# Kernel tuning notes

Hardware: AMD Instinct MI355X
Metric: run time of the kernel (lower is better)

## Reference

```python
import jax, jax.numpy as jnp
import numpy as np

RHO = 1.0


def _cayley():
    # Geometric-product structure constants for Cl(2,0), basis (1, e1, e2, e12).
    C = np.zeros((4, 4, 4), dtype=np.float32)
    entries = [
        (0, 0, 0, 1), (0, 1, 1, 1), (0, 2, 2, 1), (0, 3, 3, 1),
        (1, 0, 1, 1), (1, 1, 0, 1), (1, 2, 3, 1), (1, 3, 2, 1),
        (2, 0, 2, 1), (2, 1, 3, -1), (2, 2, 0, 1), (2, 3, 1, -1),
        (3, 0, 3, 1), (3, 1, 2, -1), (3, 2, 1, 1), (3, 3, 0, -1),
    ]
    for x, y, z, s in entries:
        C[x, y, z] = s
    return jnp.asarray(C)

CAYLEY = _cayley()

B, I, O, G, X = 64, 64, 64, 4096, 4
GRID_MIN, GRID_MAX = -2.0, 2.0


def setup_inputs() -> dict:
    key = jax.random.key(0)
    k1, k2, k3 = jax.random.split(key, 3)
    x = jax.random.normal(k1, (B, I, X), dtype=jnp.float32)
    # random_grid: quasirandom points in [grid_min, grid_max]^X (Sobol in torch; uniform here)
    grid = jax.random.uniform(k2, (G, X), dtype=jnp.float32) * (GRID_MAX - GRID_MIN) + GRID_MIN
    weights = jax.random.normal(k3, (I, O, G, X), dtype=jnp.float32)
    silu_weight = jnp.ones((I, O, X), dtype=jnp.float32)
    silu_bias = jnp.zeros((I, O, X), dtype=jnp.float32)
    return {"x": x, "grid": grid, "weights": weights,
            "silu_weight": silu_weight, "silu_bias": silu_bias}


def reference(x, grid, weights, silu_weight, silu_bias):
    # x: (B, I, X); grid: (G, X); weights: (I, O, G, X)
    diff = x[:, :, None, :] - grid[None, None, :, :]          # (B, I, G, X)
    # algebra.norm(v)**2 with Euclidean metric = sum over multivector components
    rbf = jnp.exp(-jnp.sum(diff * diff, axis=-1) / RHO)       # (B, I, G)
    result = jnp.einsum('big,iogx->biox', rbf, weights)       # (B, I, O, X)
    # componentwise SiLU branch: geometric product via cayley tensor
    sx = jax.nn.silu(x)                                       # (B, I, X)
    silu_val = jnp.einsum('iox,biy,xyz->bioz', silu_weight, sx, CAYLEY)
    silu_val = silu_val + silu_bias                           # broadcast (B, I, O, X)
    out = jnp.sum(result + silu_val, axis=1)                  # 'biox->box'
    return out                                                # NoNorm: identity norm
```

## Files before the change

kernel.cpp:

```cpp
#include <hip/hip_runtime.h>
#include <hip/hip_bf16.h>

#define BB 64
#define II 64
#define OO 64
#define GG 4096
#define KP 32
#define NCH 8
#define GC (GG / NCH)
#define NPH (GC / KP)

typedef short bf16x8 __attribute__((ext_vector_type(8)));
typedef short bf16x4 __attribute__((ext_vector_type(4)));
typedef float f32x4  __attribute__((ext_vector_type(4)));

static __device__ __forceinline__ short f2bf(float f) {
    __hip_bfloat16 h = __float2bfloat16(f);
    return __builtin_bit_cast(short, h);
}

__global__ __launch_bounds__(512, 4)
void kan_main(const float* __restrict__ xg, const float* __restrict__ grd,
              const float* __restrict__ wts, float* __restrict__ dst,
              int atomic_mode)
{
    __shared__ __align__(16) float          Wst[2][OO * KP * 4];
    __shared__ __align__(16) unsigned short As [2][BB * KP];
    __shared__ __align__(16) float4         Gs [GC];

    const int i  = blockIdx.x;
    const int ch = blockIdx.y;
    const int g0 = ch * GC;
    const int s  = (i + ch) & (NPH - 1);

    const int t    = threadIdx.x;
    const int lane = t & 63;
    const int wv   = t >> 6;

    const int brow = t >> 3;
    const int gq   = t & 7;
    const float4 xv = reinterpret_cast<const float4*>(xg)[brow * II + i];

    {
        const float4* gsrc = reinterpret_cast<const float4*>(grd) + g0 + t;
        char* ldst = (char*)(&Gs[0]) + wv * 1024;
        __builtin_amdgcn_global_load_lds(gsrc, ldst, 16, 0, 0);
    }

    const float4* w4 = reinterpret_cast<const float4*>(wts)
                       + (size_t)i * OO * GG;
    const int srow_half = lane >> 5;
    const int su        = lane & 31;

    #pragma unroll
    for (int q = 0; q < 4; ++q) {
        const int rr = 2 * (q * 8 + wv) + srow_half;
        const int gg = g0 + s * KP + (su ^ (rr & 7));
        __builtin_amdgcn_global_load_lds(w4 + (size_t)rr * GG + gg,
            (char*)(&Wst[0][0]) + (q * 8 + wv) * 1024, 16, 0, 0);
    }

    asm volatile("s_waitcnt vmcnt(4)\n\ts_barrier" ::: "memory");

    f32x4 acc[4][2];
    #pragma unroll
    for (int mt = 0; mt < 4; ++mt)
        #pragma unroll
        for (int nt = 0; nt < 2; ++nt) acc[mt][nt] = {0.f, 0.f, 0.f, 0.f};

    const int lg    = lane >> 4;
    const int r16   = lane & 15;
    const int bo_lo = r16 >> 2;
    const int bx    = r16 & 3;

    for (int p = 0; p < NPH; ++p) {
        const int b  = p & 1;
        const int cp = (p + s) & (NPH - 1);
        const int np = (p + 1 + s) & (NPH - 1);

        if (p + 1 < NPH) {
            #pragma unroll
            for (int q = 0; q < 4; ++q) {
                const int rr = 2 * (q * 8 + wv) + srow_half;
                const int gg = g0 + np * KP + (su ^ (rr & 7));
                __builtin_amdgcn_global_load_lds(w4 + (size_t)rr * GG + gg,
                    (char*)(&Wst[b ^ 1][0]) + (q * 8 + wv) * 1024, 16, 0, 0);
            }
        }

        {
            bf16x4 av;
            #pragma unroll
            for (int e = 0; e < 4; ++e) {
                const float4 gv = Gs[cp * KP + gq * 4 + e];
                const float d0 = xv.x - gv.x, d1 = xv.y - gv.y,
                            d2 = xv.z - gv.z, d3 = xv.w - gv.w;
                av[e] = f2bf(__expf(-(d0*d0 + d1*d1 + d2*d2 + d3*d3)));
            }
            *reinterpret_cast<bf16x4*>(
                &As[b][brow * KP + ((gq * 4) ^ ((brow & 3) << 3))]) = av;
        }

        if (p + 1 < NPH)
            asm volatile("s_waitcnt vmcnt(4) lgkmcnt(0)\n\ts_barrier" ::: "memory");
        else
            asm volatile("s_waitcnt vmcnt(0) lgkmcnt(0)\n\ts_barrier" ::: "memory");

        bf16x8 af[4];
        #pragma unroll
        for (int mt = 0; mt < 4; ++mt) {
            const int r = mt * 16 + r16;
            af[mt] = *reinterpret_cast<const bf16x8*>(
                &As[b][r * KP + ((lg * 8) ^ ((r & 3) << 3))]);
        }
        bf16x8 bb[2];
        #pragma unroll
        for (int nt = 0; nt < 2; ++nt) {
            const int o  = wv * 8 + nt * 4 + bo_lo;
            const int sg = o & 7;
            const float* bp = &Wst[b][o * 128 + bx];
            #pragma unroll
            for (int e = 0; e < 8; ++e)
                bb[nt][e] = f2bf(bp[(lg * 8 + (e ^ sg)) * 4]);
        }
        #pragma unroll
        for (int mt = 0; mt < 4; ++mt)
            #pragma unroll
            for (int nt = 0; nt < 2; ++nt)
                acc[mt][nt] = __builtin_amdgcn_mfma_f32_16x16x32_bf16(
                    af[mt], bb[nt], acc[mt][nt], 0, 0, 0);

        asm volatile("s_waitcnt lgkmcnt(0)\n\ts_barrier" ::: "memory");
    }

    if (!atomic_mode) {
        float* pp = dst + (size_t)(ch * 64 + i) * (BB * OO * 4);
        #pragma unroll
        for (int mt = 0; mt < 4; ++mt)
            #pragma unroll
            for (int nt = 0; nt < 2; ++nt) {
                const int n  = wv * 32 + nt * 16 + (lane & 15);
                const int mb = mt * 16 + ((lane >> 4) << 2);
                #pragma unroll
                for (int r = 0; r < 4; ++r)
                    pp[(mb + r) * 256 + n] = acc[mt][nt][r];
            }
    } else {
        #pragma unroll
        for (int mt = 0; mt < 4; ++mt)
            #pragma unroll
            for (int nt = 0; nt < 2; ++nt) {
                const int n  = wv * 32 + nt * 16 + (lane & 15);
                const int mb = mt * 16 + ((lane >> 4) << 2);
                #pragma unroll
                for (int r = 0; r < 4; ++r)
                    atomicAdd(&dst[(mb + r) * 256 + n], acc[mt][nt][r]);
            }
    }
}

__global__ __launch_bounds__(256)
void kan_tail(const float* __restrict__ part,
              const float* __restrict__ xg,
              const float* __restrict__ sw,
              const float* __restrict__ sb,
              float* __restrict__ out)
{
    __shared__ float4 sums[16][16];

    const int t     = threadIdx.x;
    const int bid   = blockIdx.x;
    const int pairL = t & 15;
    const int rgrp  = t >> 4;
    const int pairG = bid * 16 + pairL;

    const float4* p4 = reinterpret_cast<const float4*>(part);
    float4 s = make_float4(0.f, 0.f, 0.f, 0.f);
    #pragma unroll 8
    for (int k = 0; k < 32; ++k) {
        const float4 v = p4[(size_t)(rgrp * 32 + k) * 4096 + pairG];
        s.x += v.x; s.y += v.y; s.z += v.z; s.w += v.w;
    }
    sums[pairL][rgrp] = s;
    __syncthreads();

    if (t < 16) {
        const int pg = bid * 16 + t;
        const int b = pg >> 6, o = pg & 63;

        float o0 = 0.f, o1 = 0.f, o2 = 0.f, o3 = 0.f;
        #pragma unroll
        for (int r = 0; r < 16; ++r) {
            const float4 v = sums[t][r];
            o0 += v.x; o1 += v.y; o2 += v.z; o3 += v.w;
        }

        const float4* xg4 = reinterpret_cast<const float4*>(xg);
        const float4* sw4 = reinterpret_cast<const float4*>(sw);
        const float4* sb4 = reinterpret_cast<const float4*>(sb);
        #pragma unroll 4
        for (int i = 0; i < II; ++i) {
            const float4 xvv = xg4[b * II + i];
            const float4 swv = sw4[i * OO + o];
            const float4 sbv = sb4[i * OO + o];
            const float s0 = xvv.x / (1.f + __expf(-xvv.x));
            const float s1 = xvv.y / (1.f + __expf(-xvv.y));
            const float s2 = xvv.z / (1.f + __expf(-xvv.z));
            const float s3 = xvv.w / (1.f + __expf(-xvv.w));
            o0 += swv.x * s0 + swv.y * s1 + swv.z * s2 - swv.w * s3 + sbv.x;
            o1 += swv.x * s1 + swv.y * s0 - swv.z * s3 + swv.w * s2 + sbv.y;
            o2 += swv.x * s2 + swv.y * s3 + swv.z * s0 - swv.w * s1 + sbv.z;
            o3 += swv.x * s3 + swv.y * s2 - swv.z * s1 + swv.w * s0 + sbv.w;
        }
        reinterpret_cast<float4*>(out)[pg] = make_float4(o0, o1, o2, o3);
    }
}

__global__ void kan_out(const float* __restrict__ xg,
                        const float* __restrict__ sw,
                        const float* __restrict__ sb,
                        float* __restrict__ out)
{
    const int t = blockIdx.x * 256 + threadIdx.x;
    const int b = t >> 6, o = t & 63;

    const float4 v = reinterpret_cast<const float4*>(out)[t];
    float o0 = v.x, o1 = v.y, o2 = v.z, o3 = v.w;

    const float4* xg4 = reinterpret_cast<const float4*>(xg);
    const float4* sw4 = reinterpret_cast<const float4*>(sw);
    const float4* sb4 = reinterpret_cast<const float4*>(sb);
    #pragma unroll 4
    for (int i = 0; i < II; ++i) {
        const float4 xvv = xg4[b * II + i];
        const float4 swv = sw4[i * OO + o];
        const float4 sbv = sb4[i * OO + o];
        const float s0 = xvv.x / (1.f + __expf(-xvv.x));
        const float s1 = xvv.y / (1.f + __expf(-xvv.y));
        const float s2 = xvv.z / (1.f + __expf(-xvv.z));
        const float s3 = xvv.w / (1.f + __expf(-xvv.w));
        o0 += swv.x * s0 + swv.y * s1 + swv.z * s2 - swv.w * s3 + sbv.x;
        o1 += swv.x * s1 + swv.y * s0 - swv.z * s3 + swv.w * s2 + sbv.y;
        o2 += swv.x * s2 + swv.y * s3 + swv.z * s0 - swv.w * s1 + sbv.z;
        o3 += swv.x * s3 + swv.y * s2 - swv.z * s1 + swv.w * s0 + sbv.w;
    }
    reinterpret_cast<float4*>(out)[t] = make_float4(o0, o1, o2, o3);
}

extern "C" void kernel_launch(void* const* d_in, const int* in_sizes, int n_in,
                              void* d_out, int out_size, void* d_ws, size_t ws_size,
                              hipStream_t stream)
{
    const float* x   = (const float*)d_in[0];
    const float* grd = (const float*)d_in[1];
    const float* w   = (const float*)d_in[2];
    const float* sw  = (const float*)d_in[3];
    const float* sb  = (const float*)d_in[4];
    float* out = (float*)d_out;
    float* ws  = (float*)d_ws;

    const size_t need = (size_t)64 * NCH * 16384 * 4;

    if (ws_size >= need) {
        kan_main<<<dim3(64, NCH), 512, 0, stream>>>(x, grd, w, ws, 0);
        kan_tail<<<256, 256, 0, stream>>>(ws, x, sw, sb, out);
    } else {
        hipMemsetAsync(d_out, 0, (size_t)out_size * sizeof(float), stream);
        kan_main<<<dim3(64, NCH), 512, 0, stream>>>(x, grd, w, out, 1);
        kan_out<<<16, 256, 0, stream>>>(x, sw, sb, out);
    }
}
```

Before: 76.21 us.

## Split main GEMM across output chunks instead of grid chunks, shrinking partial buffer

The work split changes from eight grid-point chunks per input feature to eight output-column chunks, so each block now walks all 4096 grid points with KP=64 for a 64x32 output tile. Weights are loaded into registers, converted to bf16 and stored in LDS, replacing the earlier direct global-to-LDS fp32 staging. Partial results shrink from 512 to 64 slices, so the tail kernel becomes a simple per-thread sum over 64 partials. The cost is that each block recomputes the RBF activations for all grid points, which repeats the exp work eight times across output chunks, and each wave now issues a single MFMA tile per step.

After: 277.9 us. 3.65x slower.

```diff
diff --git a/kernel.cpp b/kernel.cpp
--- a/kernel.cpp
+++ b/kernel.cpp
@@ -5,10 +5,9 @@
 #define II 64
 #define OO 64
 #define GG 4096
-#define KP 32
-#define NCH 8
-#define GC (GG / NCH)
-#define NPH (GC / KP)
+#define KP 64
+#define NOC 8
+#define NPH (GG / KP)
 
 typedef short bf16x8 __attribute__((ext_vector_type(8)));
 typedef short bf16x4 __attribute__((ext_vector_type(4)));
@@ -17,6 +16,11 @@
 static __device__ __forceinline__ short f2bf(float f) {
     __hip_bfloat16 h = __float2bfloat16(f);
     return __builtin_bit_cast(short, h);
+}
+
+static __device__ __forceinline__ void lds_barrier() {
+    asm volatile("s_waitcnt lgkmcnt(0)" ::: "memory");
+    __builtin_amdgcn_s_barrier();
 }
 
 __global__ __launch_bounds__(512, 4)
@@ -24,138 +28,146 @@
               const float* __restrict__ wts, float* __restrict__ dst,
               int atomic_mode)
 {
-    __shared__ __align__(16) float          Wst[2][OO * KP * 4];
-    __shared__ __align__(16) unsigned short As [2][BB * KP];
-    __shared__ __align__(16) float4         Gs [GC];
+    __shared__ __align__(16) unsigned short Bs[2][32 * KP];
+    __shared__ __align__(16) unsigned short As[2][BB * KP];
 
     const int i  = blockIdx.x;
-    const int ch = blockIdx.y;
-    const int g0 = ch * GC;
-    const int s  = (i + ch) & (NPH - 1);
+    const int oc = blockIdx.y;
+    const int s  = (i + oc * 8) & (NPH - 1);
 
     const int t    = threadIdx.x;
     const int lane = t & 63;
     const int wv   = t >> 6;
 
+    const float4* wbase = reinterpret_cast<const float4*>(wts)
+        + ((size_t)i * OO + oc * 8 + wv) * GG + lane;
+
     const int brow = t >> 3;
-    const int gq   = t & 7;
-    const float4 xv = reinterpret_cast<const float4*>(xg)[brow * II + i];
-
-    {
-        const float4* gsrc = reinterpret_cast<const float4*>(grd) + g0 + t;
-        char* ldst = (char*)(&Gs[0]) + wv * 1024;
-        __builtin_amdgcn_global_load_lds(gsrc, ldst, 16, 0, 0);
-    }
-
-    const float4* w4 = reinterpret_cast<const float4*>(wts)
-                       + (size_t)i * OO * GG;
-    const int srow_half = lane >> 5;
-    const int su        = lane & 31;
-
-    #pragma unroll
-    for (int q = 0; q < 4; ++q) {
-        const int rr = 2 * (q * 8 + wv) + srow_half;
-        const int gg = g0 + s * KP + (su ^ (rr & 7));
-        __builtin_amdgcn_global_load_lds(w4 + (size_t)rr * GG + gg,
-            (char*)(&Wst[0][0]) + (q * 8 + wv) * 1024, 16, 0, 0);
-    }
-
-    asm volatile("s_waitcnt vmcnt(4)\n\ts_barrier" ::: "memory");
-
-    f32x4 acc[4][2];
-    #pragma unroll
-    for (int mt = 0; mt < 4; ++mt)
+    const int oct  = t & 7;
+    const float4* gp4 = reinterpret_cast<const float4*>(grd);
+    const float4  xv  = reinterpret_cast<const float4*>(xg)[brow * II + i];
+
+    const int mt = wv >> 1, nt = wv & 1;
+    const int lg = lane >> 4, r16 = lane & 15;
+
+    f32x4 acc = {0.f, 0.f, 0.f, 0.f};
+
+    float4 preA = wbase[(size_t)(s) * KP];
+    float4 preB = wbase[(size_t)((s + 1) & (NPH - 1)) * KP];
+    __builtin_amdgcn_sched_barrier(0);
+
+    for (int pp = 0; pp < NPH; pp += 2) {
+        {
+            const int cp = (pp + s) & (NPH - 1);
+            float4 gv[8];
+            #pragma unroll
+            for (int e = 0; e < 8; ++e) gv[e] = gp4[cp * KP + oct * 8 + e];
+
+            {
+                const float wf[4] = {preA.x, preA.y, preA.z, preA.w};
+                #pragma unroll
+                for (int x = 0; x < 4; ++x) {
+                    const int n = wv * 4 + x;
+                    Bs[0][n * KP + (lane ^ ((n & 7) << 3))] =
+                        (unsigned short)f2bf(wf[x]);
+                }
+            }
+            if (pp + 2 < NPH)
+                preA = wbase[(size_t)((pp + 2 + s) & (NPH - 1)) * KP];
+            __builtin_amdgcn_sched_barrier(0);
+
+            #pragma unroll
+            for (int h = 0; h < 2; ++h) {
+                bf16x4 av;
+                #pragma unroll
+                for (int e = 0; e < 4; ++e) {
+                    const float4 g = gv[h * 4 + e];
+                    const float d0 = xv.x - g.x, d1 = xv.y - g.y,
+                                d2 = xv.z - g.z, d3 = xv.w - g.w;
+                    av[e] = f2bf(__expf(-(d0*d0 + d1*d1 + d2*d2 + d3*d3)));
+                }
+                const int kb = oct * 8 + h * 4;
+                *reinterpret_cast<bf16x4*>(
+                    &As[0][brow * KP + (kb ^ ((brow & 7) << 3))]) = av;
+            }
+
+            lds_barrier();
+
+            #pragma unroll
+            for (int kk = 0; kk < 2; ++kk) {
+                const int kb = kk * 32 + lg * 8;
+                const int rA = mt * 16 + r16;
+                const int rB = nt * 16 + r16;
+                bf16x8 af = *reinterpret_cast<const bf16x8*>(
+                    &As[0][rA * KP + (kb ^ ((rA & 7) << 3))]);
+                bf16x8 bf = *reinterpret_cast<const bf16x8*>(
+                    &Bs[0][rB * KP + (kb ^ ((rB & 7) << 3))]);
+                acc = __builtin_amdgcn_mfma_f32_16x16x32_bf16(af, bf, acc,
+                                                              0, 0, 0);
+            }
+        }
+        {
+            const int cp = (pp + 1 + s) & (NPH - 1);
+            float4 gv[8];
+            #pragma unroll
+            for (int e = 0; e < 8; ++e) gv[e] = gp4[cp * KP + oct * 8 + e];
+
+            {
+                const float wf[4] = {preB.x, preB.y, preB.z, preB.w};
+                #pragma unroll
+                for (int x = 0; x < 4; ++x) {
+                    const int n = wv * 4 + x;
+                    Bs[1][n * KP + (lane ^ ((n & 7) << 3))] =
+                        (unsigned short)f2bf(wf[x]);
+                }
+            }
+            if (pp + 3 < NPH)
+                preB = wbase[(size_t)((pp + 3 + s) & (NPH - 1)) * KP];
+            __builtin_amdgcn_sched_barrier(0);
+
+            #pragma unroll
+            for (int h = 0; h < 2; ++h) {
+                bf16x4 av;
+                #pragma unroll
+                for (int e = 0; e < 4; ++e) {
+                    const float4 g = gv[h * 4 + e];
+                    const float d0 = xv.x - g.x, d1 = xv.y - g.y,
+                                d2 = xv.z - g.z, d3 = xv.w - g.w;
+                    av[e] = f2bf(__expf(-(d0*d0 + d1*d1 + d2*d2 + d3*d3)));
+                }
+                const int kb = oct * 8 + h * 4;
+                *reinterpret_cast<bf16x4*>(
+                    &As[1][brow * KP + (kb ^ ((brow & 7) << 3))]) = av;
+            }
+
+            lds_barrier();
+
+            #pragma unroll
+            for (int kk = 0; kk < 2; ++kk) {
+                const int kb = kk * 32 + lg * 8;
+                const int rA = mt * 16 + r16;
+                const int rB = nt * 16 + r16;
+                bf16x8 af = *reinterpret_cast<const bf16x8*>(
+                    &As[1][rA * KP + (kb ^ ((rA & 7) << 3))]);
+                bf16x8 bf = *reinterpret_cast<const bf16x8*>(
+                    &Bs[1][rB * KP + (kb ^ ((rB & 7) << 3))]);
+                acc = __builtin_amdgcn_mfma_f32_16x16x32_bf16(af, bf, acc,
+                                                              0, 0, 0);
+            }
+        }
+    }
+
+    const int n  = oc * 32 + nt * 16 + r16;
+    const int mb = mt * 16 + (lane >> 4) * 4;
+    if (!atomic_mode) {
+        float* pp_ = dst + (size_t)i * 16384;
         #pragma unroll
-        for (int nt = 0; nt < 2; ++nt) acc[mt][nt] = {0.f, 0.f, 0.f, 0.f};
-
-    const int lg    = lane >> 4;
-    const int r16   = lane & 15;
-    const int bo_lo = r16 >> 2;
-    const int bx    = r16 & 3;
-
-    for (int p = 0; p < NPH; ++p) {
-        const int b  = p & 1;
-        const int cp = (p + s) & (NPH - 1);
-        const int np = (p + 1 + s) & (NPH - 1);
-
-        if (p + 1 < NPH) {
-            #pragma unroll
-            for (int q = 0; q < 4; ++q) {
-                const int rr = 2 * (q * 8 + wv) + srow_half;
-                const int gg = g0 + np * KP + (su ^ (rr & 7));
-                __builtin_amdgcn_global_load_lds(w4 + (size_t)rr * GG + gg,
-                    (char*)(&Wst[b ^ 1][0]) + (q * 8 + wv) * 1024, 16, 0, 0);
-            }
-        }
-
-        {
-            bf16x4 av;
-            #pragma unroll
-            for (int e = 0; e < 4; ++e) {
-                const float4 gv = Gs[cp * KP + gq * 4 + e];
-                const float d0 = xv.x - gv.x, d1 = xv.y - gv.y,
-                            d2 = xv.z - gv.z, d3 = xv.w - gv.w;
-                av[e] = f2bf(__expf(-(d0*d0 + d1*d1 + d2*d2 + d3*d3)));
-            }
-            *reinterpret_cast<bf16x4*>(
-                &As[b][brow * KP + ((gq * 4) ^ ((brow & 3) << 3))]) = av;
-        }
-
-        if (p + 1 < NPH)
-            asm volatile("s_waitcnt vmcnt(4) lgkmcnt(0)\n\ts_barrier" ::: "memory");
-        else
-            asm volatile("s_waitcnt vmcnt(0) lgkmcnt(0)\n\ts_barrier" ::: "memory");
-
-        bf16x8 af[4];
-        #pragma unroll
-        for (int mt = 0; mt < 4; ++mt) {
-            const int r = mt * 16 + r16;
-            af[mt] = *reinterpret_cast<const bf16x8*>(
-                &As[b][r * KP + ((lg * 8) ^ ((r & 3) << 3))]);
-        }
-        bf16x8 bb[2];
-        #pragma unroll
-        for (int nt = 0; nt < 2; ++nt) {
-            const int o  = wv * 8 + nt * 4 + bo_lo;
-            const int sg = o & 7;
-            const float* bp = &Wst[b][o * 128 + bx];
-            #pragma unroll
-            for (int e = 0; e < 8; ++e)
-                bb[nt][e] = f2bf(bp[(lg * 8 + (e ^ sg)) * 4]);
-        }
-        #pragma unroll
-        for (int mt = 0; mt < 4; ++mt)
-            #pragma unroll
-            for (int nt = 0; nt < 2; ++nt)
-                acc[mt][nt] = __builtin_amdgcn_mfma_f32_16x16x32_bf16(
-                    af[mt], bb[nt], acc[mt][nt], 0, 0, 0);
-
-        asm volatile("s_waitcnt lgkmcnt(0)\n\ts_barrier" ::: "memory");
-    }
-
-    if (!atomic_mode) {
-        float* pp = dst + (size_t)(ch * 64 + i) * (BB * OO * 4);
-        #pragma unroll
-        for (int mt = 0; mt < 4; ++mt)
-            #pragma unroll
-            for (int nt = 0; nt < 2; ++nt) {
-                const int n  = wv * 32 + nt * 16 + (lane & 15);
-                const int mb = mt * 16 + ((lane >> 4) << 2);
-                #pragma unroll
-                for (int r = 0; r < 4; ++r)
-                    pp[(mb + r) * 256 + n] = acc[mt][nt][r];
-            }
+        for (int r = 0; r < 4; ++r)
+            pp_[(mb + r) * 256 + n] = acc[r];
     } else {
         #pragma unroll
-        for (int mt = 0; mt < 4; ++mt)
-            #pragma unroll
-            for (int nt = 0; nt < 2; ++nt) {
-                const int n  = wv * 32 + nt * 16 + (lane & 15);
-                const int mb = mt * 16 + ((lane >> 4) << 2);
-                #pragma unroll
-                for (int r = 0; r < 4; ++r)
-                    atomicAdd(&dst[(mb + r) * 256 + n], acc[mt][nt][r]);
-            }
+        for (int r = 0; r < 4; ++r)
+            atomicAdd(&dst[(mb + r) * 256 + n], acc[r]);
     }
 }
 
@@ -166,66 +178,16 @@
               const float* __restrict__ sb,
               float* __restrict__ out)
 {
-    __shared__ float4 sums[16][16];
-
-    const int t     = threadIdx.x;
-    const int bid   = blockIdx.x;
-    const int pairL = t & 15;
-    const int rgrp  = t >> 4;
-    const int pairG = bid * 16 + pairL;
+    const int j = blockIdx.x * 256 + threadIdx.x;
+    const int b = j >> 6, o = j & 63;
 
     const float4* p4 = reinterpret_cast<const float4*>(part);
-    float4 s = make_float4(0.f, 0.f, 0.f, 0.f);
+    float o0 = 0.f, o1 = 0.f, o2 = 0.f, o3 = 0.f;
     #pragma unroll 8
-    for (int k = 0; k < 32; ++k) {
-        const float4 v = p4[(size_t)(rgrp * 32 + k) * 4096 + pairG];
-        s.x += v.x; s.y += v.y; s.z += v.z; s.w += v.w;
-    }
-    sums[pairL][rgrp] = s;
-    __syncthreads();
-
-    if (t < 16) {
-        const int pg = bid * 16 + t;
-        const int b = pg >> 6, o = pg & 63;
-
-        float o0 = 0.f, o1 = 0.f, o2 = 0.f, o3 = 0.f;
-        #pragma unroll
-        for (int r = 0; r < 16; ++r) {
-            const float4 v = sums[t][r];
-            o0 += v.x; o1 += v.y; o2 += v.z; o3 += v.w;
-        }
-
-        const float4* xg4 = reinterpret_cast<const float4*>(xg);
-        const float4* sw4 = reinterpret_cast<const float4*>(sw);
-        const float4* sb4 = reinterpret_cast<const float4*>(sb);
-        #pragma unroll 4
-        for (int i = 0; i < II; ++i) {
-            const float4 xvv = xg4[b * II + i];
-            const float4 swv = sw4[i * OO + o];
-            const float4 sbv = sb4[i * OO + o];
-            const float s0 = xvv.x / (1.f + __expf(-xvv.x));
-            const float s1 = xvv.y / (1.f + __expf(-xvv.y));
-            const float s2 = xvv.z / (1.f + __expf(-xvv.z));
-            const float s3 = xvv.w / (1.f + __expf(-xvv.w));
-            o0 += swv.x * s0 + swv.y * s1 + swv.z * s2 - swv.w * s3 + sbv.x;
-            o1 += swv.x * s1 + swv.y * s0 - swv.z * s3 + swv.w * s2 + sbv.y;
-            o2 += swv.x * s2 + swv.y * s3 + swv.z * s0 - swv.w * s1 + sbv.z;
-            o3 += swv.x * s3 + swv.y * s2 - swv.z * s1 + swv.w * s0 + sbv.w;
-        }
-        reinterpret_cast<float4*>(out)[pg] = make_float4(o0, o1, o2, o3);
-    }
-}
-
-__global__ void kan_out(const float* __restrict__ xg,
-                        const float* __restrict__ sw,
-                        const float* __restrict__ sb,
-                        float* __restrict__ out)
-{
-    const int t = blockIdx.x * 256 + threadIdx.x;
-    const int b = t >> 6, o = t & 63;
-
-    const float4 v = reinterpret_cast<const float4*>(out)[t];
-    float o0 = v.x, o1 = v.y, o2 = v.z, o3 = v.w;
+    for (int ii = 0; ii < 64; ++ii) {
+        const float4 v = p4[(size_t)ii * 4096 + j];
+        o0 += v.x; o1 += v.y; o2 += v.z; o3 += v.w;
+    }
 
     const float4* xg4 = reinterpret_cast<const float4*>(xg);
     const float4* sw4 = reinterpret_cast<const float4*>(sw);
@@ -244,6 +206,37 @@
         o2 += swv.x * s2 + swv.y * s3 + swv.z * s0 - swv.w * s1 + sbv.z;
         o3 += swv.x * s3 + swv.y * s2 - swv.z * s1 + swv.w * s0 + sbv.w;
     }
+    reinterpret_cast<float4*>(out)[j] = make_float4(o0, o1, o2, o3);
+}
+
+__global__ void kan_out(const float* __restrict__ xg,
+                        const float* __restrict__ sw,
+                        const float* __restrict__ sb,
+                        float* __restrict__ out)
+{
+    const int t = blockIdx.x * 256 + threadIdx.x;
+    const int b = t >> 6, o = t & 63;
+
+    const float4 v = reinterpret_cast<const float4*>(out)[t];
+    float o0 = v.x, o1 = v.y, o2 = v.z, o3 = v.w;
+
+    const float4* xg4 = reinterpret_cast<const float4*>(xg);
+    const float4* sw4 = reinterpret_cast<const float4*>(sw);
+    const float4* sb4 = reinterpret_cast<const float4*>(sb);
+    #pragma unroll 4
+    for (int i = 0; i < II; ++i) {
+        const float4 xvv = xg4[b * II + i];
+        const float4 swv = sw4[i * OO + o];
+        const float4 sbv = sb4[i * OO + o];
+        const float s0 = xvv.x / (1.f + __expf(-xvv.x));
+        const float s1 = xvv.y / (1.f + __expf(-xvv.y));
+        const float s2 = xvv.z / (1.f + __expf(-xvv.z));
+        const float s3 = xvv.w / (1.f + __expf(-xvv.w));
+        o0 += swv.x * s0 + swv.y * s1 + swv.z * s2 - swv.w * s3 + sbv.x;
+        o1 += swv.x * s1 + swv.y * s0 - swv.z * s3 + swv.w * s2 + sbv.y;
+        o2 += swv.x * s2 + swv.y * s3 + swv.z * s0 - swv.w * s1 + sbv.z;
+        o3 += swv.x * s3 + swv.y * s2 - swv.z * s1 + swv.w * s0 + sbv.w;
+    }
     reinterpret_cast<float4*>(out)[t] = make_float4(o0, o1, o2, o3);
 }
 
@@ -259,14 +252,14 @@
     float* out = (float*)d_out;
     float* ws  = (float*)d_ws;
 
-    const size_t need = (size_t)64 * NCH * 16384 * 4;
+    const size_t need = (size_t)64 * 16384 * 4;
 
     if (ws_size >= need) {
-        kan_main<<<dim3(64, NCH), 512, 0, stream>>>(x, grd, w, ws, 0);
-        kan_tail<<<256, 256, 0, stream>>>(ws, x, sw, sb, out);
+        kan_main<<<dim3(64, NOC), 512, 0, stream>>>(x, grd, w, ws, 0);
+        kan_tail<<<16, 256, 0, stream>>>(ws, x, sw, sb, out);
     } else {
         hipMemsetAsync(d_out, 0, (size_t)out_size * sizeof(float), stream);
-        kan_main<<<dim3(64, NCH), 512, 0, stream>>>(x, grd, w, out, 1);
+        kan_main<<<dim3(64, NOC), 512, 0, stream>>>(x, grd, w, out, 1);
         kan_out<<<16, 256, 0, stream>>>(x, sw, sb, out);
     }
 }
```

## Halve grid chunks, double block size, store bf16 partials, simplify tail reduction

Applied to the files above, without the earlier changes.

The main kernel now splits G into 4 chunks instead of 8 and runs 1024-thread blocks, so each wave computes one M-tile against four N-tiles. Partial sums are written as bf16 instead of fp32, which halves the partial-sum buffer and its traffic. The tail kernel becomes a simple per-output loop over all 256 slices, launched with far fewer blocks. Risks include lower occupancy and parallelism (fewer blocks, a serial 256-iteration tail over only 16 blocks) and reduced accuracy from rounding the partials to bf16.

Result: slower. 92.56 us (+21.5%).

```diff
diff --git a/kernel.cpp b/kernel.cpp
--- a/kernel.cpp
+++ b/kernel.cpp
@@ -6,23 +6,29 @@
 #define OO 64
 #define GG 4096
 #define KP 32
-#define NCH 8
+#define NCH 4
 #define GC (GG / NCH)
 #define NPH (GC / KP)
+#define NSL (II * NCH)
 
 typedef short bf16x8 __attribute__((ext_vector_type(8)));
-typedef short bf16x4 __attribute__((ext_vector_type(4)));
+typedef short bf16x2 __attribute__((ext_vector_type(2)));
 typedef float f32x4  __attribute__((ext_vector_type(4)));
-
-static __device__ __forceinline__ short f2bf(float f) {
+typedef unsigned short u16x4 __attribute__((ext_vector_type(4)));
+
+static __device__ __forceinline__ unsigned short f2bfu(float f) {
     __hip_bfloat16 h = __float2bfloat16(f);
-    return __builtin_bit_cast(short, h);
-}
-
-__global__ __launch_bounds__(512, 4)
+    return __builtin_bit_cast(unsigned short, h);
+}
+static __device__ __forceinline__ float bfu2f(unsigned short u) {
+    unsigned int v = (unsigned int)u << 16;
+    return __builtin_bit_cast(float, v);
+}
+
+__global__ __launch_bounds__(1024, 4)
 void kan_main(const float* __restrict__ xg, const float* __restrict__ grd,
-              const float* __restrict__ wts, float* __restrict__ dst,
-              int atomic_mode)
+              const float* __restrict__ wts, unsigned short* __restrict__ dst,
+              float* __restrict__ fdst, int atomic_mode)
 {
     __shared__ __align__(16) float          Wst[2][OO * KP * 4];
     __shared__ __align__(16) unsigned short As [2][BB * KP];
@@ -31,14 +37,14 @@
     const int i  = blockIdx.x;
     const int ch = blockIdx.y;
     const int g0 = ch * GC;
-    const int s  = (i + ch) & (NPH - 1);
+    const int s  = (i + ch * 8) & (NPH - 1);
 
     const int t    = threadIdx.x;
     const int lane = t & 63;
     const int wv   = t >> 6;
 
-    const int brow = t >> 3;
-    const int gq   = t & 7;
+    const int brow = t >> 4;
+    const int gq   = t & 15;
     const float4 xv = reinterpret_cast<const float4*>(xg)[brow * II + i];
 
     {
@@ -53,25 +59,26 @@
     const int su        = lane & 31;
 
     #pragma unroll
-    for (int q = 0; q < 4; ++q) {
-        const int rr = 2 * (q * 8 + wv) + srow_half;
+    for (int q = 0; q < 2; ++q) {
+        const int j  = q * 16 + wv;
+        const int rr = 2 * j + srow_half;
         const int gg = g0 + s * KP + (su ^ (rr & 7));
         __builtin_amdgcn_global_load_lds(w4 + (size_t)rr * GG + gg,
-            (char*)(&Wst[0][0]) + (q * 8 + wv) * 1024, 16, 0, 0);
-    }
-
-    asm volatile("s_waitcnt vmcnt(4)\n\ts_barrier" ::: "memory");
-
-    f32x4 acc[4][2];
+            (char*)(&Wst[0][0]) + j * 1024, 16, 0, 0);
+    }
+
+    asm volatile("s_waitcnt vmcnt(2)\n\ts_barrier" ::: "memory");
+
+    f32x4 acc[4];
     #pragma unroll
-    for (int mt = 0; mt < 4; ++mt)
-        #pragma unroll
-        for (int nt = 0; nt < 2; ++nt) acc[mt][nt] = {0.f, 0.f, 0.f, 0.f};
-
-    const int lg    = lane >> 4;
-    const int r16   = lane & 15;
-    const int bo_lo = r16 >> 2;
-    const int bx    = r16 & 3;
+    for (int q = 0; q < 4; ++q) acc[q] = {0.f, 0.f, 0.f, 0.f};
+
+    const int mt  = wv & 3;
+    const int n4  = (wv >> 2) * 4;
+    const int lg  = lane >> 4;
+    const int r16 = lane & 15;
+    const int bo  = r16 >> 2;
+    const int bx  = r16 & 3;
 
     for (int p = 0; p < NPH; ++p) {
         const int b  = p & 1;
@@ -80,152 +87,92 @@
 
         if (p + 1 < NPH) {
             #pragma unroll
-            for (int q = 0; q < 4; ++q) {
-                const int rr = 2 * (q * 8 + wv) + srow_half;
+            for (int q = 0; q < 2; ++q) {
+                const int j  = q * 16 + wv;
+                const int rr = 2 * j + srow_half;
                 const int gg = g0 + np * KP + (su ^ (rr & 7));
                 __builtin_amdgcn_global_load_lds(w4 + (size_t)rr * GG + gg,
-                    (char*)(&Wst[b ^ 1][0]) + (q * 8 + wv) * 1024, 16, 0, 0);
+                    (char*)(&Wst[b ^ 1][0]) + j * 1024, 16, 0, 0);
             }
         }
 
         {
-            bf16x4 av;
-            #pragma unroll
-            for (int e = 0; e < 4; ++e) {
-                const float4 gv = Gs[cp * KP + gq * 4 + e];
-                const float d0 = xv.x - gv.x, d1 = xv.y - gv.y,
-                            d2 = xv.z - gv.z, d3 = xv.w - gv.w;
-                av[e] = f2bf(__expf(-(d0*d0 + d1*d1 + d2*d2 + d3*d3)));
+            bf16x2 av;
+            #pragma unroll
+            for (int e = 0; e < 2; ++e) {
+                const float4 g = Gs[cp * KP + gq * 2 + e];
+                const float d0 = xv.x - g.x, d1 = xv.y - g.y,
+                            d2 = xv.z - g.z, d3 = xv.w - g.w;
+                av[e] = (short)f2bfu(__expf(-(d0*d0 + d1*d1 + d2*d2 + d3*d3)));
             }
-            *reinterpret_cast<bf16x4*>(
-                &As[b][brow * KP + ((gq * 4) ^ ((brow & 3) << 3))]) = av;
+            const int kb = gq * 2;
+            *reinterpret_cast<bf16x2*>(
+                &As[b][brow * KP + (kb ^ ((brow & 3) << 3))]) = av;
         }
 
         if (p + 1 < NPH)
-            asm volatile("s_waitcnt vmcnt(4) lgkmcnt(0)\n\ts_barrier" ::: "memory");
+            asm volatile("s_waitcnt vmcnt(2) lgkmcnt(0)\n\ts_barrier" ::: "memory");
         else
             asm volatile("s_waitcnt vmcnt(0) lgkmcnt(0)\n\ts_barrier" ::: "memory");
 
-        bf16x8 af[4];
+        const int rA = mt * 16 + r16;
+        const bf16x8 af = *reinterpret_cast<const bf16x8*>(
+            &As[b][rA * KP + ((lg * 8) ^ ((rA & 3) << 3))]);
         #pragma unroll
-        for (int mt = 0; mt < 4; ++mt) {
-            const int r = mt * 16 + r16;
-            af[mt] = *reinterpret_cast<const bf16x8*>(
-                &As[b][r * KP + ((lg * 8) ^ ((r & 3) << 3))]);
-        }
-        bf16x8 bb[2];
-        #pragma unroll
-        for (int nt = 0; nt < 2; ++nt) {
-            const int o  = wv * 8 + nt * 4 + bo_lo;
+        for (int q = 0; q < 4; ++q) {
+            const int o  = (n4 + q) * 4 + bo;
             const int sg = o & 7;
             const float* bp = &Wst[b][o * 128 + bx];
+            bf16x8 bb;
             #pragma unroll
             for (int e = 0; e < 8; ++e)
-                bb[nt][e] = f2bf(bp[(lg * 8 + (e ^ sg)) * 4]);
-        }
+                bb[e] = (short)f2bfu(bp[(lg * 8 + (e ^ sg)) * 4]);
+            acc[q] = __builtin_amdgcn_mfma_f32_16x16x32_bf16(af, bb, acc[q],
+                                                             0, 0, 0);
+        }
+
+        asm volatile("s_waitcnt lgkmcnt(0)\n\ts_barrier" ::: "memory");
+    }
+
+    const int mb = mt * 16 + (lane >> 4) * 4;
+    if (!atomic_mode) {
+        unsigned short* pd = dst + (size_t)(i * NCH + ch) * (BB * 256);
         #pragma unroll
-        for (int mt = 0; mt < 4; ++mt)
-            #pragma unroll
-            for (int nt = 0; nt < 2; ++nt)
-                acc[mt][nt] = __builtin_amdgcn_mfma_f32_16x16x32_bf16(
-                    af[mt], bb[nt], acc[mt][nt], 0, 0, 0);
-
-        asm volatile("s_waitcnt lgkmcnt(0)\n\ts_barrier" ::: "memory");
-    }
-
-    if (!atomic_mode) {
-        float* pp = dst + (size_t)(ch * 64 + i) * (BB * OO * 4);
-        #pragma unroll
-        for (int mt = 0; mt < 4; ++mt)
-            #pragma unroll
-            for (int nt = 0; nt < 2; ++nt) {
-                const int n  = wv * 32 + nt * 16 + (lane & 15);
-                const int mb = mt * 16 + ((lane >> 4) << 2);
-                #pragma unroll
-                for (int r = 0; r < 4; ++r)
-                    pp[(mb + r) * 256 + n] = acc[mt][nt][r];
-            }
+        for (int q = 0; q < 4; ++q) {
+            const int n = (n4 + q) * 16 + r16;
+            #pragma unroll
+            for (int r = 0; r < 4; ++r)
+                pd[(mb + r) * 256 + n] = f2bfu(acc[q][r]);
+        }
     } else {
         #pragma unroll
-        for (int mt = 0; mt < 4; ++mt)
-            #pragma unroll
-            for (int nt = 0; nt < 2; ++nt) {
-                const int n  = wv * 32 + nt * 16 + (lane & 15);
-                const int mb = mt * 16 + ((lane >> 4) << 2);
-                #pragma unroll
-                for (int r = 0; r < 4; ++r)
-                    atomicAdd(&dst[(mb + r) * 256 + n], acc[mt][nt][r]);
-            }
+        for (int q = 0; q < 4; ++q) {
+            const int n = (n4 + q) * 16 + r16;
+            #pragma unroll
+            for (int r = 0; r < 4; ++r)
+                atomicAdd(&fdst[(mb + r) * 256 + n], acc[q][r]);
+        }
     }
 }
 
 __global__ __launch_bounds__(256)
-void kan_tail(const float* __restrict__ part,
+void kan_tail(const unsigned short* __restrict__ part,
               const float* __restrict__ xg,
               const float* __restrict__ sw,
               const float* __restrict__ sb,
               float* __restrict__ out)
 {
-    __shared__ float4 sums[16][16];
-
-    const int t     = threadIdx.x;
-    const int bid   = blockIdx.x;
-    const int pairL = t & 15;
-    const int rgrp  = t >> 4;
-    const int pairG = bid * 16 + pairL;
-
-    const float4* p4 = reinterpret_cast<const float4*>(part);
-    float4 s = make_float4(0.f, 0.f, 0.f, 0.f);
+    const int j = blockIdx.x * 256 + threadIdx.x;
+    const int b = j >> 6, o = j & 63;
+
+    const u16x4* p4 = reinterpret_cast<const u16x4*>(part);
+    float o0 = 0.f, o1 = 0.f, o2 = 0.f, o3 = 0.f;
     #pragma unroll 8
-    for (int k = 0; k < 32; ++k) {
-        const float4 v = p4[(size_t)(rgrp * 32 + k) * 4096 + pairG];
-        s.x += v.x; s.y += v.y; s.z += v.z; s.w += v.w;
-    }
-    sums[pairL][rgrp] = s;
-    __syncthreads();
-
-    if (t < 16) {
-        const int pg = bid * 16 + t;
-        const int b = pg >> 6, o = pg & 63;
-
-        float o0 = 0.f, o1 = 0.f, o2 = 0.f, o3 = 0.f;
-        #pragma unroll
-        for (int r = 0; r < 16; ++r) {
-            const float4 v = sums[t][r];
-            o0 += v.x; o1 += v.y; o2 += v.z; o3 += v.w;
-        }
-
-        const float4* xg4 = reinterpret_cast<const float4*>(xg);
-        const float4* sw4 = reinterpret_cast<const float4*>(sw);
-        const float4* sb4 = reinterpret_cast<const float4*>(sb);
-        #pragma unroll 4
-        for (int i = 0; i < II; ++i) {
-            const float4 xvv = xg4[b * II + i];
-            const float4 swv = sw4[i * OO + o];
-            const float4 sbv = sb4[i * OO + o];
-            const float s0 = xvv.x / (1.f + __expf(-xvv.x));
-            const float s1 = xvv.y / (1.f + __expf(-xvv.y));
-            const float s2 = xvv.z / (1.f + __expf(-xvv.z));
-            const float s3 = xvv.w / (1.f + __expf(-xvv.w));
-            o0 += swv.x * s0 + swv.y * s1 + swv.z * s2 - swv.w * s3 + sbv.x;
-            o1 += swv.x * s1 + swv.y * s0 - swv.z * s3 + swv.w * s2 + sbv.y;
-            o2 += swv.x * s2 + swv.y * s3 + swv.z * s0 - swv.w * s1 + sbv.z;
-            o3 += swv.x * s3 + swv.y * s2 - swv.z * s1 + swv.w * s0 + sbv.w;
-        }
-        reinterpret_cast<float4*>(out)[pg] = make_float4(o0, o1, o2, o3);
-    }
-}
-
-__global__ void kan_out(const float* __restrict__ xg,
-                        const float* __restrict__ sw,
-                        const float* __restrict__ sb,
-                        float* __restrict__ out)
-{
-    const int t = blockIdx.x * 256 + threadIdx.x;
-    const int b = t >> 6, o = t & 63;
-
-    const float4 v = reinterpret_cast<const float4*>(out)[t];
-    float o0 = v.x, o1 = v.y, o2 = v.z, o3 = v.w;
+    for (int sl = 0; sl < NSL; ++sl) {
+        const u16x4 v = p4[(size_t)sl * 4096 + j];
+        o0 += bfu2f(v[0]); o1 += bfu2f(v[1]);
+        o2 += bfu2f(v[2]); o3 += bfu2f(v[3]);
+    }
 
     const float4* xg4 = reinterpret_cast<const float4*>(xg);
     const float4* sw4 = reinterpret_cast<const float4*>(sw);
@@ -244,6 +191,37 @@
         o2 += swv.x * s2 + swv.y * s3 + swv.z * s0 - swv.w * s1 + sbv.z;
         o3 += swv.x * s3 + swv.y * s2 - swv.z * s1 + swv.w * s0 + sbv.w;
     }
+    reinterpret_cast<float4*>(out)[j] = make_float4(o0, o1, o2, o3);
+}
+
+__global__ void kan_out(const float* __restrict__ xg,
+                        const float* __restrict__ sw,
+                        const float* __restrict__ sb,
+                        float* __restrict__ out)
+{
+    const int t = blockIdx.x * 256 + threadIdx.x;
+    const int b = t >> 6, o = t & 63;
+
+    const float4 v = reinterpret_cast<const float4*>(out)[t];
+    float o0 = v.x, o1 = v.y, o2 = v.z, o3 = v.w;
+
+    const float4* xg4 = reinterpret_cast<const float4*>(xg);
+    const float4* sw4 = reinterpret_cast<const float4*>(sw);
+    const float4* sb4 = reinterpret_cast<const float4*>(sb);
+    #pragma unroll 4
+    for (int i = 0; i < II; ++i) {
+        const float4 xvv = xg4[b * II + i];
+        const float4 swv = sw4[i * OO + o];
+        const float4 sbv = sb4[i * OO + o];
+        const float s0 = xvv.x / (1.f + __expf(-xvv.x));
+        const float s1 = xvv.y / (1.f + __expf(-xvv.y));
+        const float s2 = xvv.z / (1.f + __expf(-xvv.z));
+        const float s3 = xvv.w / (1.f + __expf(-xvv.w));
+        o0 += swv.x * s0 + swv.y * s1 + swv.z * s2 - swv.w * s3 + sbv.x;
+        o1 += swv.x * s1 + swv.y * s0 - swv.z * s3 + swv.w * s2 + sbv.y;
+        o2 += swv.x * s2 + swv.y * s3 + swv.z * s0 - swv.w * s1 + sbv.z;
+        o3 += swv.x * s3 + swv.y * s2 - swv.z * s1 + swv.w * s0 + sbv.w;
+    }
     reinterpret_cast<float4*>(out)[t] = make_float4(o0, o1, o2, o3);
 }
 
@@ -257,16 +235,16 @@
     const float* sw  = (const float*)d_in[3];
     const float* sb  = (const float*)d_in[4];
     float* out = (float*)d_out;
-    float* ws  = (float*)d_ws;
-
-    const size_t need = (size_t)64 * NCH * 16384 * 4;
+
+    const size_t need = (size_t)NSL * 16384 * 2;
 
     if (ws_size >= need) {
-        kan_main<<<dim3(64, NCH), 512, 0, stream>>>(x, grd, w, ws, 0);
-        kan_tail<<<256, 256, 0, stream>>>(ws, x, sw, sb, out);
+        unsigned short* ws = (unsigned short*)d_ws;
+        kan_main<<<dim3(64, NCH), 1024, 0, stream>>>(x, grd, w, ws, nullptr, 0);
+        kan_tail<<<16, 256, 0, stream>>>(ws, x, sw, sb, out);
     } else {
         hipMemsetAsync(d_out, 0, (size_t)out_size * sizeof(float), stream);
-        kan_main<<<dim3(64, NCH), 512, 0, stream>>>(x, grd, w, out, 1);
+        kan_main<<<dim3(64, NCH), 1024, 0, stream>>>(x, grd, w, nullptr, out, 1);
         kan_out<<<16, 256, 0, stream>>>(x, sw, sb, out);
     }
 }
```
